# Optimization experiments

Hardware: AMD Instinct MI355X
Metric: run time of the kernel (lower is better)

The kernel has to match this reference:

```python
import jax, jax.numpy as jnp
import numpy as np

B, L, D, H = 2, 2048, 1024, 16
DK = D // H


def setup_inputs() -> dict:
    key = jax.random.key(0)
    ks = jax.random.split(key, 13)
    s = 1.0 / np.sqrt(D)
    return {
        "q": jax.random.normal(ks[0], (B, L, D), jnp.float32),
        "k": jax.random.normal(ks[1], (B, L, D), jnp.float32),
        "v": jax.random.normal(ks[2], (B, L, D), jnp.float32),
        "mask": jax.random.randint(ks[3], (B, L, L), 0, 2, jnp.int32),
        "Wq": jax.random.normal(ks[4], (D, D), jnp.float32) * s,
        "bq": jnp.zeros((D,), jnp.float32),
        "Wk": jax.random.normal(ks[5], (D, D), jnp.float32) * s,
        "bk": jnp.zeros((D,), jnp.float32),
        "Wv": jax.random.normal(ks[6], (D, D), jnp.float32) * s,
        "bv": jnp.zeros((D,), jnp.float32),
        "Wo": jax.random.normal(ks[7], (D, D), jnp.float32) * s,
        "bo": jnp.zeros((D,), jnp.float32),
    }


def reference(q, k, v, mask, Wq, bq, Wk, bk, Wv, bv, Wo, bo):
    # projections: [B, L, D] -> [B, L, H, DK]
    qh = (q @ Wq + bq).reshape(B, L, H, DK)
    kh = (k @ Wk + bk).reshape(B, L, H, DK)
    vh = (v @ Wv + bv).reshape(B, L, H, DK)
    # scores scaled by d_model (module passes model_dim=d_model, not sqrt(d_k))
    attn = jnp.einsum("bqhd,bkhd->bhqk", qh, kh) / D
    attn = jnp.where(mask[:, None, :, :] == 0, jnp.float32(-1e9), attn)
    attn = jax.nn.softmax(attn, axis=-1)  # [B, H, Lq, Lk]
    ctx = jnp.einsum("bhqk,bkhd->bqhd", attn, vh)  # [B, Lq, H, DK]
    out = ctx.reshape(B, L, D) @ Wo + bo
    # original returns attn flattened head-major: [H*B, Lq, Lk]
    attn_out = attn.transpose(1, 0, 2, 3).reshape(H * B, L, L)
    return out, attn_out
```

## Files before the change

### kernel.cpp

```cpp
#include <hip/hip_runtime.h>
#include <cstdint>

typedef unsigned short u16;
typedef unsigned long long u64;
typedef __attribute__((ext_vector_type(8))) short short8;
typedef __attribute__((ext_vector_type(4))) float floatx4;

#define DEV __device__ __forceinline__

#define GLD16(gp, lp)                                                          \
  __builtin_amdgcn_global_load_lds(                                            \
      (const __attribute__((address_space(1))) void*)(gp),                     \
      (__attribute__((address_space(3))) void*)(lp), 16, 0, 0)

DEV u16 f2bf(float f) {
  union { float f; uint32_t u; } x; x.f = f;
  uint32_t r = x.u + 0x7fffu + ((x.u >> 16) & 1u);
  return (u16)(r >> 16);
}


__global__ __launch_bounds__(256) void cvt_bf16(
    const float* __restrict__ src, u16* __restrict__ dst) {
  int i = (blockIdx.x * 256 + threadIdx.x) * 4;
  float4 v = *(const float4*)(src + i);
  ushort4 o;
  o.x = f2bf(v.x); o.y = f2bf(v.y); o.z = f2bf(v.z); o.w = f2bf(v.w);
  *(ushort4*)(dst + i) = o;
}

__global__ __launch_bounds__(256) void pack_mask(
    const int* __restrict__ mask, u64* __restrict__ mw) {
  const int lane = threadIdx.x & 63;
  int gw = (blockIdx.x * 256 + threadIdx.x) >> 6;
  const int nwaves = (gridDim.x * 256) >> 6;
  const int total = (2 * 2048 * 2048) / 64;
  for (int c = gw; c < total; c += nwaves) {
    int v = mask[(size_t)c * 64 + lane];
    u64 b = __ballot(v != 0);
    if (lane == 0) mw[c] = b;
  }
}

__global__ __launch_bounds__(256) void transpose_w(
    const float* __restrict__ s0, const float* __restrict__ s1,
    const float* __restrict__ s2, const float* __restrict__ s3,
    u16* __restrict__ d0, u16* __restrict__ d1,
    u16* __restrict__ d2, u16* __restrict__ d3) {
  const float* S; u16* D;
  switch (blockIdx.z) {
    case 0: S = s0; D = d0; break;
    case 1: S = s1; D = d1; break;
    case 2: S = s2; D = d2; break;
    default: S = s3; D = d3; break;
  }
  __shared__ u16 t[64][68];
  const int tid = threadIdx.x;
  const int r0 = blockIdx.y * 64, c0 = blockIdx.x * 64;
#pragma unroll
  for (int i = 0; i < 4; ++i) {
    int idx = i * 256 + tid;
    int r = idx >> 4, c = (idx & 15) * 4;
    float4 v = *(const float4*)(S + (size_t)(r0 + r) * 1024 + c0 + c);
    t[r][c] = f2bf(v.x); t[r][c + 1] = f2bf(v.y);
    t[r][c + 2] = f2bf(v.z); t[r][c + 3] = f2bf(v.w);
  }
  __syncthreads();
#pragma unroll
  for (int i = 0; i < 4; ++i) {
    int idx = i * 256 + tid;
    int r = idx >> 4, c = (idx & 15) * 4;
    ushort4 v;
    v.x = t[c][r]; v.y = t[c + 1][r]; v.z = t[c + 2][r]; v.w = t[c + 3][r];
    *(ushort4*)(D + (size_t)(c0 + r) * 1024 + r0 + c) = v;
  }
}

__global__ __launch_bounds__(256) void gemm128(
    const u16* __restrict__ X, const u16* __restrict__ Wt,
    const float* __restrict__ bias, u16* __restrict__ outb,
    float* __restrict__ outf, int mode) {
  __shared__ __align__(16) u16 As[128 * 32];
  __shared__ __align__(16) u16 Bs[128 * 32];
  const int tid = threadIdx.x;
  const int wave = tid >> 6, lane = tid & 63;
  const int quad = lane >> 4, l16 = lane & 15;
  const int wm = (wave >> 1) * 64, wn = (wave & 1) * 64;
  const int m0 = blockIdx.x * 128, n0 = blockIdx.y * 128;

  floatx4 acc[4][4];
#pragma unroll
  for (int i = 0; i < 4; ++i)
#pragma unroll
    for (int j = 0; j < 4; ++j) acc[i][j] = (floatx4){0.f, 0.f, 0.f, 0.f};

  for (int k0 = 0; k0 < 1024; k0 += 32) {
#pragma unroll
    for (int r = 0; r < 2; ++r) {
      int c = r * 256 + tid;
      int row = c >> 2, off = (c & 3) * 8;
      GLD16(X + (size_t)(m0 + row) * 1024 + k0 + off, As + c * 8);
      GLD16(Wt + (size_t)(n0 + row) * 1024 + k0 + off, Bs + c * 8);
    }
    __syncthreads();
    short8 a[4], b[4];
#pragma unroll
    for (int i = 0; i < 4; ++i)
      a[i] = *(const short8*)(As + (wm + i * 16 + l16) * 32 + quad * 8);
#pragma unroll
    for (int i = 0; i < 4; ++i)
      b[i] = *(const short8*)(Bs + (wn + i * 16 + l16) * 32 + quad * 8);
#pragma unroll
    for (int mi = 0; mi < 4; ++mi)
#pragma unroll
      for (int ni = 0; ni < 4; ++ni)
        acc[mi][ni] = __builtin_amdgcn_mfma_f32_16x16x32_bf16(
            a[mi], b[ni], acc[mi][ni], 0, 0, 0);
    __syncthreads();
  }

#pragma unroll
  for (int mi = 0; mi < 4; ++mi) {
#pragma unroll
    for (int ni = 0; ni < 4; ++ni) {
      const int gn = n0 + wn + ni * 16 + l16;
      const float bv = bias[gn];
#pragma unroll
      for (int reg = 0; reg < 4; ++reg) {
        const int gm = m0 + wm + mi * 16 + quad * 4 + reg;
        const float v = acc[mi][ni][reg] + bv;
        if (mode == 2) {
          outf[(size_t)gm * 1024 + gn] = v;
        } else {
          int bb = gm >> 11, l = gm & 2047, hh = gn >> 6, dk = gn & 63;
          size_t addr = (mode == 0)
              ? (((size_t)(bb * 16 + hh) * 2048 + l) * 64 + dk)
              : (((size_t)(bb * 16 + hh) * 64 + dk) * 2048 + l);
          outb[addr] = f2bf(v);
        }
      }
    }
  }
}

__global__ __launch_bounds__(256) void rowsum_k(
    const u16* __restrict__ qh, const u16* __restrict__ kh,
    const u64* __restrict__ mw, float* __restrict__ rowinv) {
  const int tid = threadIdx.x;
  const int wave = tid >> 6, lane = tid & 63;
  const int quad = lane >> 4, l16 = lane & 15;
  const int q0 = blockIdx.x * 64, h = blockIdx.y, b = blockIdx.z;
  const int bh = b * 16 + h;

  __shared__ __align__(16) u16 Qs[64 * 72];
  __shared__ __align__(16) u16 Ks[128 * 72];
  __shared__ float red[4][64];

  const u16* qbase = qh + ((size_t)bh * 2048 + q0) * 64;
  const u16* kbase = kh + (size_t)bh * 2048 * 64;
  const u64* mwrow = mw + ((size_t)b * 2048 + q0) * 32;

#pragma unroll
  for (int r = 0; r < 2; ++r) {
    int c = r * 256 + tid;
    int row = c >> 3, off = (c & 7) * 8;
    uint4 v = *(const uint4*)(qbase + (size_t)c * 8);
    *(uint4*)(Qs + row * 72 + off) = v;
  }

  float rs[4][4];
#pragma unroll
  for (int i = 0; i < 4; ++i)
#pragma unroll
    for (int j = 0; j < 4; ++j) rs[i][j] = 0.f;

  for (int kt = 0; kt < 16; ++kt) {
#pragma unroll
    for (int r = 0; r < 4; ++r) {
      int c = r * 256 + tid;
      int row = c >> 3, off = (c & 7) * 8;
      uint4 v = *(const uint4*)(kbase + (size_t)kt * 8192 + c * 8);
      *(uint4*)(Ks + row * 72 + off) = v;
    }
    __syncthreads();

    floatx4 s[4][2];
#pragma unroll
    for (int i = 0; i < 4; ++i) {
      s[i][0] = (floatx4){0.f, 0.f, 0.f, 0.f};
      s[i][1] = (floatx4){0.f, 0.f, 0.f, 0.f};
    }
#pragma unroll
    for (int kk = 0; kk < 64; kk += 32) {
      short8 a[4], bb[2];
#pragma unroll
      for (int i = 0; i < 4; ++i)
        a[i] = *(const short8*)(Qs + (i * 16 + l16) * 72 + kk + quad * 8);
#pragma unroll
      for (int j = 0; j < 2; ++j)
        bb[j] = *(const short8*)(Ks + (wave * 32 + j * 16 + l16) * 72 + kk + quad * 8);
#pragma unroll
      for (int mi = 0; mi < 4; ++mi)
#pragma unroll
        for (int ni = 0; ni < 2; ++ni)
          s[mi][ni] = __builtin_amdgcn_mfma_f32_16x16x32_bf16(
              a[mi], bb[ni], s[mi][ni], 0, 0, 0);
    }
#pragma unroll
    for (int mi = 0; mi < 4; ++mi)
#pragma unroll
      for (int reg = 0; reg < 4; ++reg) {
        int row = mi * 16 + quad * 4 + reg;
        u64 w = mwrow[row * 32 + kt * 2 + (wave >> 1)];
#pragma unroll
        for (int ni = 0; ni < 2; ++ni) {
          int bit = (wave & 1) * 32 + ni * 16 + l16;
          float sv = s[mi][ni][reg] * (1.0f / 1024.0f);
          rs[mi][reg] += ((w >> bit) & 1) ? __expf(sv) : 0.f;
        }
      }
    __syncthreads();
  }

#pragma unroll
  for (int mi = 0; mi < 4; ++mi)
#pragma unroll
    for (int reg = 0; reg < 4; ++reg) {
      float v = rs[mi][reg];
      v += __shfl_xor(v, 1, 64);
      v += __shfl_xor(v, 2, 64);
      v += __shfl_xor(v, 4, 64);
      v += __shfl_xor(v, 8, 64);
      rs[mi][reg] = v;
    }
  if (l16 == 0) {
#pragma unroll
    for (int mi = 0; mi < 4; ++mi)
#pragma unroll
      for (int reg = 0; reg < 4; ++reg)
        red[wave][mi * 16 + quad * 4 + reg] = rs[mi][reg];
  }
  __syncthreads();
  if (tid < 64) {
    float sum = red[0][tid] + red[1][tid] + red[2][tid] + red[3][tid];
    rowinv[(size_t)bh * 2048 + q0 + tid] = (sum > 0.f) ? (1.0f / sum) : -1.0f;
  }
}

__global__ __launch_bounds__(256) void attn_k(
    const u16* __restrict__ qh, const u16* __restrict__ kh,
    const u16* __restrict__ vt, const u64* __restrict__ mw,
    const float* __restrict__ rowinv, float* __restrict__ attn_out,
    u16* __restrict__ ctx) {
  const int tid = threadIdx.x;
  const int wave = tid >> 6, lane = tid & 63;
  const int quad = lane >> 4, l16 = lane & 15;
  const int q0 = blockIdx.x * 64, h = blockIdx.y, b = blockIdx.z;
  const int bh = b * 16 + h;

  __shared__ __align__(16) u16 Qs[64 * 72];
  __shared__ __align__(16) u16 Ks[128 * 72];
  __shared__ __align__(16) u16 Vs[64 * 136];
  __shared__ __align__(16) u16 Ps[64 * 136];

  const u16* qbase = qh + ((size_t)bh * 2048 + q0) * 64;
  const u16* kbase = kh + (size_t)bh * 2048 * 64;
  const u16* vbase = vt + (size_t)bh * 64 * 2048;
  const u64* mwrow = mw + ((size_t)b * 2048 + q0) * 32;
  float* abase = attn_out + ((size_t)(h * 2 + b) * 2048 + q0) * 2048;

#pragma unroll
  for (int r = 0; r < 2; ++r) {
    int c = r * 256 + tid;
    int row = c >> 3, off = (c & 7) * 8;
    uint4 v = *(const uint4*)(qbase + (size_t)c * 8);
    *(uint4*)(Qs + row * 72 + off) = v;
  }

  float inv[4][4];
#pragma unroll
  for (int mi = 0; mi < 4; ++mi)
#pragma unroll
    for (int reg = 0; reg < 4; ++reg)
      inv[mi][reg] = rowinv[(size_t)bh * 2048 + q0 + mi * 16 + quad * 4 + reg];

  floatx4 cacc[4];
#pragma unroll
  for (int i = 0; i < 4; ++i) cacc[i] = (floatx4){0.f, 0.f, 0.f, 0.f};

  for (int kt = 0; kt < 16; ++kt) {
#pragma unroll
    for (int r = 0; r < 4; ++r) {
      int c = r * 256 + tid;
      int row = c >> 3, off = (c & 7) * 8;
      uint4 v = *(const uint4*)(kbase + (size_t)kt * 8192 + c * 8);
      *(uint4*)(Ks + row * 72 + off) = v;
      int dk = c >> 4, ko = (c & 15) * 8;
      uint4 w = *(const uint4*)(vbase + (size_t)dk * 2048 + kt * 128 + ko);
      *(uint4*)(Vs + dk * 136 + ko) = w;
    }
    __syncthreads();

    floatx4 s[4][2];
#pragma unroll
    for (int i = 0; i < 4; ++i) {
      s[i][0] = (floatx4){0.f, 0.f, 0.f, 0.f};
      s[i][1] = (floatx4){0.f, 0.f, 0.f, 0.f};
    }
#pragma unroll
    for (int kk = 0; kk < 64; kk += 32) {
      short8 a[4], bb[2];
#pragma unroll
      for (int i = 0; i < 4; ++i)
        a[i] = *(const short8*)(Qs + (i * 16 + l16) * 72 + kk + quad * 8);
#pragma unroll
      for (int j = 0; j < 2; ++j)
        bb[j] = *(const short8*)(Ks + (wave * 32 + j * 16 + l16) * 72 + kk + quad * 8);
#pragma unroll
      for (int mi = 0; mi < 4; ++mi)
#pragma unroll
        for (int ni = 0; ni < 2; ++ni)
          s[mi][ni] = __builtin_amdgcn_mfma_f32_16x16x32_bf16(
              a[mi], bb[ni], s[mi][ni], 0, 0, 0);
    }

#pragma unroll
    for (int mi = 0; mi < 4; ++mi)
#pragma unroll
      for (int reg = 0; reg < 4; ++reg) {
        int row = mi * 16 + quad * 4 + reg;
        u64 w = mwrow[row * 32 + kt * 2 + (wave >> 1)];
        float iv = inv[mi][reg];
#pragma unroll
        for (int ni = 0; ni < 2; ++ni) {
          int keyl = wave * 32 + ni * 16 + l16;
          int key = kt * 128 + keyl;
          int bit = (wave & 1) * 32 + ni * 16 + l16;
          float sv = s[mi][ni][reg] * (1.0f / 1024.0f);
          float p = (iv < 0.f) ? (1.0f / 2048.0f)
                               : (((w >> bit) & 1) ? __expf(sv) * iv : 0.f);
          abase[(size_t)row * 2048 + key] = p;
          Ps[row * 136 + keyl] = f2bf(p);
        }
      }
    __syncthreads();

#pragma unroll
    for (int ks = 0; ks < 4; ++ks) {
      short8 a[4];
#pragma unroll
      for (int mi = 0; mi < 4; ++mi)
        a[mi] = *(const short8*)(Ps + (mi * 16 + l16) * 136 + ks * 32 + quad * 8);
      short8 bb = *(const short8*)(Vs + (wave * 16 + l16) * 136 + ks * 32 + quad * 8);
#pragma unroll
      for (int mi = 0; mi < 4; ++mi)
        cacc[mi] = __builtin_amdgcn_mfma_f32_16x16x32_bf16(a[mi], bb, cacc[mi], 0, 0, 0);
    }
    __syncthreads();
  }

#pragma unroll
  for (int mi = 0; mi < 4; ++mi)
#pragma unroll
    for (int reg = 0; reg < 4; ++reg) {
      int row = q0 + mi * 16 + quad * 4 + reg;
      int col = h * 64 + wave * 16 + l16;
      ctx[(size_t)(b * 2048 + row) * 1024 + col] = f2bf(cacc[mi][reg]);
    }
}

extern "C" void kernel_launch(void* const* d_in, const int* in_sizes, int n_in,
                              void* d_out, int out_size, void* d_ws, size_t ws_size,
                              hipStream_t stream) {
  const float* q    = (const float*)d_in[0];
  const float* k    = (const float*)d_in[1];
  const float* v    = (const float*)d_in[2];
  const int*   mask = (const int*)d_in[3];
  const float* Wq   = (const float*)d_in[4];
  const float* bq   = (const float*)d_in[5];
  const float* Wk   = (const float*)d_in[6];
  const float* bk   = (const float*)d_in[7];
  const float* Wv   = (const float*)d_in[8];
  const float* bv   = (const float*)d_in[9];
  const float* Wo   = (const float*)d_in[10];
  const float* bo   = (const float*)d_in[11];

  float* out  = (float*)d_out;
  float* attn = out + (size_t)4096 * 1024;

  const size_t M = 1u << 20;
  u16* wtq = (u16*)d_ws;
  u16* wtk = wtq + M;
  u16* wtv = wtk + M;
  u16* wto = wtv + M;
  u16* xb  = wto + M;
  u16* qh  = xb + 4 * M;
  u16* kh  = qh + 4 * M;
  u16* vt  = kh + 4 * M;
  u16* ctx = xb;
  float* rinv = (float*)(vt + 4 * M);
  u64* mw = (u64*)(rinv + 64 * 1024);

  pack_mask<<<dim3(512), 256, 0, stream>>>(mask, mw);
  transpose_w<<<dim3(16, 16, 4), 256, 0, stream>>>(Wq, Wk, Wv, Wo, wtq, wtk, wtv, wto);

  cvt_bf16<<<dim3(4096), 256, 0, stream>>>(q, xb);
  gemm128<<<dim3(32, 8), 256, 0, stream>>>(xb, wtq, bq, qh, nullptr, 0);
  cvt_bf16<<<dim3(4096), 256, 0, stream>>>(k, xb);
  gemm128<<<dim3(32, 8), 256, 0, stream>>>(xb, wtk, bk, kh, nullptr, 0);
  cvt_bf16<<<dim3(4096), 256, 0, stream>>>(v, xb);
  gemm128<<<dim3(32, 8), 256, 0, stream>>>(xb, wtv, bv, vt, nullptr, 1);

  rowsum_k<<<dim3(32, 16, 2), 256, 0, stream>>>(qh, kh, mw, rinv);
  attn_k<<<dim3(32, 16, 2), 256, 0, stream>>>(qh, kh, vt, mw, rinv, attn, ctx);
  gemm128<<<dim3(32, 8), 256, 0, stream>>>(ctx, wto, bo, nullptr, out, 2);
}
```

Measured before the change: 955.8 us.

## Batch QKV projections, fuse rowsum into attention, swap MFMA operands, remap blocks to XCDs

Merges the three bf16 conversions and the three QKV projection GEMMs into single batched launches. It folds the row-sum pass into the attention kernel so the row inverse stays in shared memory instead of a separate launch and buffer. It also transposes the QK^T MFMA operand order so each lane holds four consecutive keys, enabling vectorized nontemporal float4 stores of the attention matrix and ushort4 LDS writes. GEMM K-tiles grow from 32 to 64, and block indices are remapped so neighbouring tiles land on the same XCD for L2 reuse. The risks are higher LDS use and register pressure (launch bounds of 3 and 2 blocks) and a larger workspace.

```diff
diff --git a/kernel.cpp b/kernel.cpp
--- a/kernel.cpp
+++ b/kernel.cpp
@@ -19,15 +19,6 @@
   return (u16)(r >> 16);
 }
 
-
-__global__ __launch_bounds__(256) void cvt_bf16(
-    const float* __restrict__ src, u16* __restrict__ dst) {
-  int i = (blockIdx.x * 256 + threadIdx.x) * 4;
-  float4 v = *(const float4*)(src + i);
-  ushort4 o;
-  o.x = f2bf(v.x); o.y = f2bf(v.y); o.z = f2bf(v.z); o.w = f2bf(v.w);
-  *(ushort4*)(dst + i) = o;
-}
 
 __global__ __launch_bounds__(256) void pack_mask(
     const int* __restrict__ mask, u64* __restrict__ mw) {
@@ -76,17 +67,53 @@
   }
 }
 
-__global__ __launch_bounds__(256) void gemm128(
-    const u16* __restrict__ X, const u16* __restrict__ Wt,
-    const float* __restrict__ bias, u16* __restrict__ outb,
-    float* __restrict__ outf, int mode) {
-  __shared__ __align__(16) u16 As[128 * 32];
-  __shared__ __align__(16) u16 Bs[128 * 32];
+__global__ __launch_bounds__(256) void cvt3(
+    const float* __restrict__ q, const float* __restrict__ k,
+    const float* __restrict__ v, u16* __restrict__ dst) {
+  const float* S = (blockIdx.z == 0) ? q : (blockIdx.z == 1) ? k : v;
+  u16* D = dst + (size_t)blockIdx.z * (4u << 20);
+  int i = (blockIdx.x * 256 + threadIdx.x) * 4;
+  float4 val = *(const float4*)(S + i);
+  ushort4 o;
+  o.x = f2bf(val.x); o.y = f2bf(val.y); o.z = f2bf(val.z); o.w = f2bf(val.w);
+  *(ushort4*)(D + i) = o;
+}
+
+__global__ __launch_bounds__(256, 3) void gemm_k(
+    const u16* xb3, const u16* wts,
+    const float* __restrict__ bq, const float* __restrict__ bk,
+    const float* __restrict__ bv, const float* __restrict__ bo,
+    u16* __restrict__ qh, u16* __restrict__ kh, u16* __restrict__ vt,
+    const u16* ctx, float* __restrict__ out, int phase) {
+  __shared__ __align__(16) u16 As[128 * 64];
+  __shared__ __align__(16) u16 Bs[128 * 64];
   const int tid = threadIdx.x;
   const int wave = tid >> 6, lane = tid & 63;
   const int quad = lane >> 4, l16 = lane & 15;
   const int wm = (wave >> 1) * 64, wn = (wave & 1) * 64;
-  const int m0 = blockIdx.x * 128, n0 = blockIdx.y * 128;
+
+  int m0, n0, mode;
+  const u16 *X, *Wt; const float* bias;
+  u16* outb; float* outf;
+  if (phase == 0) {
+    int flat = blockIdx.x + 32 * (blockIdx.y + 8 * blockIdx.z);
+    int xcd = flat & 7, idx = flat >> 3;
+    int g = xcd * 3 + (idx >> 5);
+    int z = g >> 3;
+    m0 = (idx & 31) * 128; n0 = (g & 7) * 128;
+    X = xb3 + (size_t)z * (4u << 20);
+    Wt = wts + (size_t)z * (1u << 20);
+    bias = (z == 0) ? bq : (z == 1) ? bk : bv;
+    outb = (z == 0) ? qh : (z == 1) ? kh : vt;
+    outf = nullptr;
+    mode = (z == 2) ? 1 : 0;
+  } else {
+    int flat = blockIdx.x + 32 * blockIdx.y;
+    int xcd = flat & 7, idx = flat >> 3;
+    m0 = (xcd * 4 + (idx >> 3)) * 128; n0 = (idx & 7) * 128;
+    X = ctx; Wt = wts + 3 * (size_t)(1u << 20);
+    bias = bo; outb = nullptr; outf = out; mode = 2;
+  }
 
   floatx4 acc[4][4];
 #pragma unroll
@@ -94,28 +121,31 @@
 #pragma unroll
     for (int j = 0; j < 4; ++j) acc[i][j] = (floatx4){0.f, 0.f, 0.f, 0.f};
 
-  for (int k0 = 0; k0 < 1024; k0 += 32) {
-#pragma unroll
-    for (int r = 0; r < 2; ++r) {
+  for (int k0 = 0; k0 < 1024; k0 += 64) {
+#pragma unroll
+    for (int r = 0; r < 4; ++r) {
       int c = r * 256 + tid;
-      int row = c >> 2, off = (c & 3) * 8;
+      int row = c >> 3, off = (c & 7) * 8;
       GLD16(X + (size_t)(m0 + row) * 1024 + k0 + off, As + c * 8);
       GLD16(Wt + (size_t)(n0 + row) * 1024 + k0 + off, Bs + c * 8);
     }
     __syncthreads();
-    short8 a[4], b[4];
-#pragma unroll
-    for (int i = 0; i < 4; ++i)
-      a[i] = *(const short8*)(As + (wm + i * 16 + l16) * 32 + quad * 8);
-#pragma unroll
-    for (int i = 0; i < 4; ++i)
-      b[i] = *(const short8*)(Bs + (wn + i * 16 + l16) * 32 + quad * 8);
-#pragma unroll
-    for (int mi = 0; mi < 4; ++mi)
-#pragma unroll
-      for (int ni = 0; ni < 4; ++ni)
-        acc[mi][ni] = __builtin_amdgcn_mfma_f32_16x16x32_bf16(
-            a[mi], b[ni], acc[mi][ni], 0, 0, 0);
+#pragma unroll
+    for (int kk = 0; kk < 64; kk += 32) {
+      short8 a[4], b[4];
+#pragma unroll
+      for (int i = 0; i < 4; ++i)
+        a[i] = *(const short8*)(As + (wm + i * 16 + l16) * 64 + kk + quad * 8);
+#pragma unroll
+      for (int i = 0; i < 4; ++i)
+        b[i] = *(const short8*)(Bs + (wn + i * 16 + l16) * 64 + kk + quad * 8);
+#pragma unroll
+      for (int mi = 0; mi < 4; ++mi)
+#pragma unroll
+        for (int ni = 0; ni < 4; ++ni)
+          acc[mi][ni] = __builtin_amdgcn_mfma_f32_16x16x32_bf16(
+              a[mi], b[ni], acc[mi][ni], 0, 0, 0);
+    }
     __syncthreads();
   }
 
@@ -124,13 +154,13 @@
 #pragma unroll
     for (int ni = 0; ni < 4; ++ni) {
       const int gn = n0 + wn + ni * 16 + l16;
-      const float bv = bias[gn];
+      const float bv_ = bias[gn];
 #pragma unroll
       for (int reg = 0; reg < 4; ++reg) {
         const int gm = m0 + wm + mi * 16 + quad * 4 + reg;
-        const float v = acc[mi][ni][reg] + bv;
+        const float v = acc[mi][ni][reg] + bv_;
         if (mode == 2) {
-          outf[(size_t)gm * 1024 + gn] = v;
+          __builtin_nontemporal_store(v, outf + (size_t)gm * 1024 + gn);
         } else {
           int bb = gm >> 11, l = gm & 2047, hh = gn >> 6, dk = gn & 63;
           size_t addr = (mode == 0)
@@ -143,125 +173,27 @@
   }
 }
 
-__global__ __launch_bounds__(256) void rowsum_k(
+__global__ __launch_bounds__(256, 2) void attn_fused(
     const u16* __restrict__ qh, const u16* __restrict__ kh,
-    const u64* __restrict__ mw, float* __restrict__ rowinv) {
+    const u16* __restrict__ vt, const u64* __restrict__ mw,
+    float* __restrict__ attn_out, u16* __restrict__ ctx) {
   const int tid = threadIdx.x;
   const int wave = tid >> 6, lane = tid & 63;
   const int quad = lane >> 4, l16 = lane & 15;
-  const int q0 = blockIdx.x * 64, h = blockIdx.y, b = blockIdx.z;
-  const int bh = b * 16 + h;
-
-  __shared__ __align__(16) u16 Qs[64 * 72];
-  __shared__ __align__(16) u16 Ks[128 * 72];
-  __shared__ float red[4][64];
-
-  const u16* qbase = qh + ((size_t)bh * 2048 + q0) * 64;
-  const u16* kbase = kh + (size_t)bh * 2048 * 64;
-  const u64* mwrow = mw + ((size_t)b * 2048 + q0) * 32;
-
-#pragma unroll
-  for (int r = 0; r < 2; ++r) {
-    int c = r * 256 + tid;
-    int row = c >> 3, off = (c & 7) * 8;
-    uint4 v = *(const uint4*)(qbase + (size_t)c * 8);
-    *(uint4*)(Qs + row * 72 + off) = v;
-  }
-
-  float rs[4][4];
-#pragma unroll
-  for (int i = 0; i < 4; ++i)
-#pragma unroll
-    for (int j = 0; j < 4; ++j) rs[i][j] = 0.f;
-
-  for (int kt = 0; kt < 16; ++kt) {
-#pragma unroll
-    for (int r = 0; r < 4; ++r) {
-      int c = r * 256 + tid;
-      int row = c >> 3, off = (c & 7) * 8;
-      uint4 v = *(const uint4*)(kbase + (size_t)kt * 8192 + c * 8);
-      *(uint4*)(Ks + row * 72 + off) = v;
-    }
-    __syncthreads();
-
-    floatx4 s[4][2];
-#pragma unroll
-    for (int i = 0; i < 4; ++i) {
-      s[i][0] = (floatx4){0.f, 0.f, 0.f, 0.f};
-      s[i][1] = (floatx4){0.f, 0.f, 0.f, 0.f};
-    }
-#pragma unroll
-    for (int kk = 0; kk < 64; kk += 32) {
-      short8 a[4], bb[2];
-#pragma unroll
-      for (int i = 0; i < 4; ++i)
-        a[i] = *(const short8*)(Qs + (i * 16 + l16) * 72 + kk + quad * 8);
-#pragma unroll
-      for (int j = 0; j < 2; ++j)
-        bb[j] = *(const short8*)(Ks + (wave * 32 + j * 16 + l16) * 72 + kk + quad * 8);
-#pragma unroll
-      for (int mi = 0; mi < 4; ++mi)
-#pragma unroll
-        for (int ni = 0; ni < 2; ++ni)
-          s[mi][ni] = __builtin_amdgcn_mfma_f32_16x16x32_bf16(
-              a[mi], bb[ni], s[mi][ni], 0, 0, 0);
-    }
-#pragma unroll
-    for (int mi = 0; mi < 4; ++mi)
-#pragma unroll
-      for (int reg = 0; reg < 4; ++reg) {
-        int row = mi * 16 + quad * 4 + reg;
-        u64 w = mwrow[row * 32 + kt * 2 + (wave >> 1)];
-#pragma unroll
-        for (int ni = 0; ni < 2; ++ni) {
-          int bit = (wave & 1) * 32 + ni * 16 + l16;
-          float sv = s[mi][ni][reg] * (1.0f / 1024.0f);
-          rs[mi][reg] += ((w >> bit) & 1) ? __expf(sv) : 0.f;
-        }
-      }
-    __syncthreads();
-  }
-
-#pragma unroll
-  for (int mi = 0; mi < 4; ++mi)
-#pragma unroll
-    for (int reg = 0; reg < 4; ++reg) {
-      float v = rs[mi][reg];
-      v += __shfl_xor(v, 1, 64);
-      v += __shfl_xor(v, 2, 64);
-      v += __shfl_xor(v, 4, 64);
-      v += __shfl_xor(v, 8, 64);
-      rs[mi][reg] = v;
-    }
-  if (l16 == 0) {
-#pragma unroll
-    for (int mi = 0; mi < 4; ++mi)
-#pragma unroll
-      for (int reg = 0; reg < 4; ++reg)
-        red[wave][mi * 16 + quad * 4 + reg] = rs[mi][reg];
-  }
-  __syncthreads();
-  if (tid < 64) {
-    float sum = red[0][tid] + red[1][tid] + red[2][tid] + red[3][tid];
-    rowinv[(size_t)bh * 2048 + q0 + tid] = (sum > 0.f) ? (1.0f / sum) : -1.0f;
-  }
-}
-
-__global__ __launch_bounds__(256) void attn_k(
-    const u16* __restrict__ qh, const u16* __restrict__ kh,
-    const u16* __restrict__ vt, const u64* __restrict__ mw,
-    const float* __restrict__ rowinv, float* __restrict__ attn_out,
-    u16* __restrict__ ctx) {
-  const int tid = threadIdx.x;
-  const int wave = tid >> 6, lane = tid & 63;
-  const int quad = lane >> 4, l16 = lane & 15;
-  const int q0 = blockIdx.x * 64, h = blockIdx.y, b = blockIdx.z;
+
+  const int flat = blockIdx.x + 32 * (blockIdx.y + 16 * blockIdx.z);
+  const int xcd = flat & 7, idx = flat >> 3;
+  const int hb = xcd * 4 + (idx >> 5);
+  const int q0 = (idx & 31) * 64;
+  const int h = hb & 15, b = hb >> 4;
   const int bh = b * 16 + h;
 
   __shared__ __align__(16) u16 Qs[64 * 72];
   __shared__ __align__(16) u16 Ks[128 * 72];
   __shared__ __align__(16) u16 Vs[64 * 136];
   __shared__ __align__(16) u16 Ps[64 * 136];
+  __shared__ float red[4][64];
+  __shared__ float rinvs[64];
 
   const u16* qbase = qh + ((size_t)bh * 2048 + q0) * 64;
   const u16* kbase = kh + (size_t)bh * 2048 * 64;
@@ -273,76 +205,144 @@
   for (int r = 0; r < 2; ++r) {
     int c = r * 256 + tid;
     int row = c >> 3, off = (c & 7) * 8;
-    uint4 v = *(const uint4*)(qbase + (size_t)c * 8);
-    *(uint4*)(Qs + row * 72 + off) = v;
-  }
-
-  float inv[4][4];
-#pragma unroll
-  for (int mi = 0; mi < 4; ++mi)
-#pragma unroll
-    for (int reg = 0; reg < 4; ++reg)
-      inv[mi][reg] = rowinv[(size_t)bh * 2048 + q0 + mi * 16 + quad * 4 + reg];
-
-  floatx4 cacc[4];
-#pragma unroll
-  for (int i = 0; i < 4; ++i) cacc[i] = (floatx4){0.f, 0.f, 0.f, 0.f};
+    uint4 vv = *(const uint4*)(qbase + (size_t)c * 8);
+    *(uint4*)(Qs + row * 72 + off) = vv;
+  }
+
+  float rs[4] = {0.f, 0.f, 0.f, 0.f};
 
   for (int kt = 0; kt < 16; ++kt) {
 #pragma unroll
     for (int r = 0; r < 4; ++r) {
       int c = r * 256 + tid;
       int row = c >> 3, off = (c & 7) * 8;
-      uint4 v = *(const uint4*)(kbase + (size_t)kt * 8192 + c * 8);
-      *(uint4*)(Ks + row * 72 + off) = v;
-      int dk = c >> 4, ko = (c & 15) * 8;
-      uint4 w = *(const uint4*)(vbase + (size_t)dk * 2048 + kt * 128 + ko);
-      *(uint4*)(Vs + dk * 136 + ko) = w;
-    }
-    __syncthreads();
-
-    floatx4 s[4][2];
-#pragma unroll
-    for (int i = 0; i < 4; ++i) {
-      s[i][0] = (floatx4){0.f, 0.f, 0.f, 0.f};
-      s[i][1] = (floatx4){0.f, 0.f, 0.f, 0.f};
-    }
+      uint4 vv = *(const uint4*)(kbase + (size_t)kt * 8192 + c * 8);
+      *(uint4*)(Ks + row * 72 + off) = vv;
+    }
+    __syncthreads();
+
+    floatx4 st[2][4];
+#pragma unroll
+    for (int i = 0; i < 2; ++i)
+#pragma unroll
+      for (int j = 0; j < 4; ++j) st[i][j] = (floatx4){0.f, 0.f, 0.f, 0.f};
 #pragma unroll
     for (int kk = 0; kk < 64; kk += 32) {
-      short8 a[4], bb[2];
-#pragma unroll
-      for (int i = 0; i < 4; ++i)
-        a[i] = *(const short8*)(Qs + (i * 16 + l16) * 72 + kk + quad * 8);
-#pragma unroll
-      for (int j = 0; j < 2; ++j)
-        bb[j] = *(const short8*)(Ks + (wave * 32 + j * 16 + l16) * 72 + kk + quad * 8);
-#pragma unroll
-      for (int mi = 0; mi < 4; ++mi)
-#pragma unroll
-        for (int ni = 0; ni < 2; ++ni)
-          s[mi][ni] = __builtin_amdgcn_mfma_f32_16x16x32_bf16(
-              a[mi], bb[ni], s[mi][ni], 0, 0, 0);
-    }
-
-#pragma unroll
-    for (int mi = 0; mi < 4; ++mi)
-#pragma unroll
-      for (int reg = 0; reg < 4; ++reg) {
-        int row = mi * 16 + quad * 4 + reg;
-        u64 w = mwrow[row * 32 + kt * 2 + (wave >> 1)];
-        float iv = inv[mi][reg];
-#pragma unroll
-        for (int ni = 0; ni < 2; ++ni) {
-          int keyl = wave * 32 + ni * 16 + l16;
-          int key = kt * 128 + keyl;
-          int bit = (wave & 1) * 32 + ni * 16 + l16;
-          float sv = s[mi][ni][reg] * (1.0f / 1024.0f);
-          float p = (iv < 0.f) ? (1.0f / 2048.0f)
-                               : (((w >> bit) & 1) ? __expf(sv) * iv : 0.f);
-          abase[(size_t)row * 2048 + key] = p;
-          Ps[row * 136 + keyl] = f2bf(p);
+      short8 a[2], bqf[4];
+#pragma unroll
+      for (int ki = 0; ki < 2; ++ki)
+        a[ki] = *(const short8*)(Ks + (wave * 32 + ki * 16 + l16) * 72 + kk + quad * 8);
+#pragma unroll
+      for (int qi = 0; qi < 4; ++qi)
+        bqf[qi] = *(const short8*)(Qs + (qi * 16 + l16) * 72 + kk + quad * 8);
+#pragma unroll
+      for (int ki = 0; ki < 2; ++ki)
+#pragma unroll
+        for (int qi = 0; qi < 4; ++qi)
+          st[ki][qi] = __builtin_amdgcn_mfma_f32_16x16x32_bf16(
+              a[ki], bqf[qi], st[ki][qi], 0, 0, 0);
+    }
+
+#pragma unroll
+    for (int qi = 0; qi < 4; ++qi) {
+      u64 w = mwrow[(size_t)(qi * 16 + l16) * 32 + kt * 2 + (wave >> 1)];
+#pragma unroll
+      for (int ki = 0; ki < 2; ++ki) {
+        int bb0 = (wave & 1) * 32 + ki * 16 + quad * 4;
+#pragma unroll
+        for (int reg = 0; reg < 4; ++reg) {
+          float sv = st[ki][qi][reg] * (1.0f / 1024.0f);
+          rs[qi] += ((w >> (bb0 + reg)) & 1) ? __expf(sv) : 0.f;
         }
       }
+    }
+    __syncthreads();
+  }
+
+#pragma unroll
+  for (int qi = 0; qi < 4; ++qi) {
+    float vsum = rs[qi];
+    vsum += __shfl_xor(vsum, 16, 64);
+    vsum += __shfl_xor(vsum, 32, 64);
+    rs[qi] = vsum;
+  }
+  if (quad == 0) {
+#pragma unroll
+    for (int qi = 0; qi < 4; ++qi) red[wave][qi * 16 + l16] = rs[qi];
+  }
+  __syncthreads();
+  if (tid < 64) {
+    float s = red[0][tid] + red[1][tid] + red[2][tid] + red[3][tid];
+    rinvs[tid] = (s > 0.f) ? (1.0f / s) : -1.0f;
+  }
+  __syncthreads();
+
+  float inv[4];
+#pragma unroll
+  for (int qi = 0; qi < 4; ++qi) inv[qi] = rinvs[qi * 16 + l16];
+
+  floatx4 cacc[4];
+#pragma unroll
+  for (int i = 0; i < 4; ++i) cacc[i] = (floatx4){0.f, 0.f, 0.f, 0.f};
+
+  for (int kt = 0; kt < 16; ++kt) {
+#pragma unroll
+    for (int r = 0; r < 4; ++r) {
+      int c = r * 256 + tid;
+      int row = c >> 3, off = (c & 7) * 8;
+      uint4 vv = *(const uint4*)(kbase + (size_t)kt * 8192 + c * 8);
+      *(uint4*)(Ks + row * 72 + off) = vv;
+      int dk = c >> 4, ko = (c & 15) * 8;
+      uint4 wv = *(const uint4*)(vbase + (size_t)dk * 2048 + kt * 128 + ko);
+      *(uint4*)(Vs + dk * 136 + ko) = wv;
+    }
+    __syncthreads();
+
+    floatx4 st[2][4];
+#pragma unroll
+    for (int i = 0; i < 2; ++i)
+#pragma unroll
+      for (int j = 0; j < 4; ++j) st[i][j] = (floatx4){0.f, 0.f, 0.f, 0.f};
+#pragma unroll
+    for (int kk = 0; kk < 64; kk += 32) {
+      short8 a[2], bqf[4];
+#pragma unroll
+      for (int ki = 0; ki < 2; ++ki)
+        a[ki] = *(const short8*)(Ks + (wave * 32 + ki * 16 + l16) * 72 + kk + quad * 8);
+#pragma unroll
+      for (int qi = 0; qi < 4; ++qi)
+        bqf[qi] = *(const short8*)(Qs + (qi * 16 + l16) * 72 + kk + quad * 8);
+#pragma unroll
+      for (int ki = 0; ki < 2; ++ki)
+#pragma unroll
+        for (int qi = 0; qi < 4; ++qi)
+          st[ki][qi] = __builtin_amdgcn_mfma_f32_16x16x32_bf16(
+              a[ki], bqf[qi], st[ki][qi], 0, 0, 0);
+    }
+
+#pragma unroll
+    for (int qi = 0; qi < 4; ++qi) {
+      int row = qi * 16 + l16;
+      u64 w = mwrow[(size_t)row * 32 + kt * 2 + (wave >> 1)];
+      float iv = inv[qi];
+#pragma unroll
+      for (int ki = 0; ki < 2; ++ki) {
+        int bb0 = (wave & 1) * 32 + ki * 16 + quad * 4;
+        int keyl = wave * 32 + ki * 16 + quad * 4;
+        floatx4 pv; ushort4 pb;
+#pragma unroll
+        for (int reg = 0; reg < 4; ++reg) {
+          float sv = st[ki][qi][reg] * (1.0f / 1024.0f);
+          float p = (iv < 0.f) ? (1.0f / 2048.0f)
+                               : (((w >> (bb0 + reg)) & 1) ? __expf(sv) * iv : 0.f);
+          pv[reg] = p;
+          ((u16*)&pb)[reg] = f2bf(p);
+        }
+        __builtin_nontemporal_store(
+            pv, (floatx4*)(abase + (size_t)row * 2048 + kt * 128 + keyl));
+        *(ushort4*)(Ps + row * 136 + keyl) = pb;
+      }
+    }
     __syncthreads();
 
 #pragma unroll
@@ -393,25 +393,20 @@
   u16* wtk = wtq + M;
   u16* wtv = wtk + M;
   u16* wto = wtv + M;
-  u16* xb  = wto + M;
-  u16* qh  = xb + 4 * M;
+  u16* xb3 = wto + M;
+  u16* qh  = xb3 + 12 * M;
   u16* kh  = qh + 4 * M;
   u16* vt  = kh + 4 * M;
-  u16* ctx = xb;
-  float* rinv = (float*)(vt + 4 * M);
-  u64* mw = (u64*)(rinv + 64 * 1024);
+  u64* mw  = (u64*)(vt + 4 * M);
+  u16* ctx = xb3;
 
   pack_mask<<<dim3(512), 256, 0, stream>>>(mask, mw);
   transpose_w<<<dim3(16, 16, 4), 256, 0, stream>>>(Wq, Wk, Wv, Wo, wtq, wtk, wtv, wto);
-
-  cvt_bf16<<<dim3(4096), 256, 0, stream>>>(q, xb);
-  gemm128<<<dim3(32, 8), 256, 0, stream>>>(xb, wtq, bq, qh, nullptr, 0);
-  cvt_bf16<<<dim3(4096), 256, 0, stream>>>(k, xb);
-  gemm128<<<dim3(32, 8), 256, 0, stream>>>(xb, wtk, bk, kh, nullptr, 0);
-  cvt_bf16<<<dim3(4096), 256, 0, stream>>>(v, xb);
-  gemm128<<<dim3(32, 8), 256, 0, stream>>>(xb, wtv, bv, vt, nullptr, 1);
-
-  rowsum_k<<<dim3(32, 16, 2), 256, 0, stream>>>(qh, kh, mw, rinv);
-  attn_k<<<dim3(32, 16, 2), 256, 0, stream>>>(qh, kh, vt, mw, rinv, attn, ctx);
-  gemm128<<<dim3(32, 8), 256, 0, stream>>>(ctx, wto, bo, nullptr, out, 2);
-}
+  cvt3<<<dim3(4096, 1, 3), 256, 0, stream>>>(q, k, v, xb3);
+
+  gemm_k<<<dim3(32, 8, 3), 256, 0, stream>>>(xb3, wtq, bq, bk, bv, bo,
+                                             qh, kh, vt, ctx, out, 0);
+  attn_fused<<<dim3(32, 16, 2), 256, 0, stream>>>(qh, kh, vt, mw, attn, ctx);
+  gemm_k<<<dim3(32, 8, 1), 256, 0, stream>>>(xb3, wtq, bq, bk, bv, bo,
+                                             qh, kh, vt, ctx, out, 1);
+}
```

New measurement: 844.7 us. 11.6% less time.
